# Kernel optimization log

Hardware: AMD Instinct MI355X
Metric: run time of the kernel (lower is better)

Reference implementation:

```python
import jax, jax.numpy as jnp
import numpy as np

L, H, E, DK, FF, V, BS = 6, 16, 1024, 64, 4096, 32000, 1024
B, T = 2, 1024
EPS = 1e-5


def _ln(x, g, b):
    mu = jnp.mean(x, axis=-1, keepdims=True)
    var = jnp.mean(jnp.square(x - mu), axis=-1, keepdims=True)
    return (x - mu) * jax.lax.rsqrt(var + EPS) * g + b


def setup_inputs() -> dict:
    key = jax.random.key(0)
    ks = jax.random.split(key, 12)
    s = 0.02
    return {
        'idx': jax.random.randint(ks[0], (B, T), 0, V),
        'emb': jax.random.normal(ks[1], (V, E), jnp.float32) * s,
        'pos': jax.random.normal(ks[2], (BS, E), jnp.float32) * s,
        'Wq': jax.random.normal(ks[3], (L, H, E, DK), jnp.float32) * s,
        'Wk': jax.random.normal(ks[4], (L, H, E, DK), jnp.float32) * s,
        'Wv': jax.random.normal(ks[5], (L, H, E, DK), jnp.float32) * s,
        'Wp': jax.random.normal(ks[6], (L, E, E), jnp.float32) * s,
        'bp': jnp.zeros((L, E), jnp.float32),
        'ln1_g': jnp.ones((L, E), jnp.float32),
        'ln1_b': jnp.zeros((L, E), jnp.float32),
        'ln2_g': jnp.ones((L, E), jnp.float32),
        'ln2_b': jnp.zeros((L, E), jnp.float32),
        'W1': jax.random.normal(ks[7], (L, E, FF), jnp.float32) * s,
        'b1': jnp.zeros((L, FF), jnp.float32),
        'W2': jax.random.normal(ks[8], (L, FF, E), jnp.float32) * s,
        'b2': jnp.zeros((L, E), jnp.float32),
        'lnf_g': jnp.ones((E,), jnp.float32),
        'lnf_b': jnp.zeros((E,), jnp.float32),
        'Wout': jax.random.normal(ks[9], (E, V), jnp.float32) * s,
        'bout': jnp.zeros((V,), jnp.float32),
    }


def reference(idx, emb, pos, Wq, Wk, Wv, Wp, bp, ln1_g, ln1_b, ln2_g, ln2_b,
              W1, b1, W2, b2, lnf_g, lnf_b, Wout, bout):
    Tcur = idx.shape[1]
    x = emb[idx] + pos[:Tcur]  # [B,T,E]
    # NOTE: original code scales by 1/sqrt(n_embd) (input dim), NOT 1/sqrt(d_k)
    scale = 1.0 / jnp.sqrt(jnp.float32(E))
    causal = jnp.tril(jnp.ones((Tcur, Tcur), bool))
    neg_inf = jnp.float32(-jnp.inf)
    for l in range(L):
        h = _ln(x, ln1_g[l], ln1_b[l])
        q = jnp.einsum('bte,hed->bhtd', h, Wq[l])
        k = jnp.einsum('bte,hed->bhtd', h, Wk[l])
        v = jnp.einsum('bte,hed->bhtd', h, Wv[l])
        scores = jnp.einsum('bhtd,bhsd->bhts', q, k) * scale
        scores = jnp.where(causal, scores, neg_inf)
        attn = jax.nn.softmax(scores, axis=-1)
        o = jnp.einsum('bhts,bhsd->bhtd', attn, v)
        o = o.transpose(0, 2, 1, 3).reshape(x.shape[0], Tcur, H * DK)
        x = x + o @ Wp[l] + bp[l]
        h = _ln(x, ln2_g[l], ln2_b[l])
        x = x + jax.nn.relu(h @ W1[l] + b1[l]) @ W2[l] + b2[l]
    x = _ln(x, lnf_g, lnf_b)
    logits = x @ Wout + bout  # [B,T,V]
    return logits
```

## Files before the change

### kernel.cpp

```cpp
#include <hip/hip_runtime.h>
#include <cstdio>
#include <cstdint>

typedef unsigned short u16;
typedef __bf16 bf16x8 __attribute__((ext_vector_type(8)));
typedef float f32x4 __attribute__((ext_vector_type(4)));

static const int EE = 1024;
static const int TT = 1024;
static const int BB = 2;
static const int NTOK = 2048;
static const int HH = 16;
static const int DK = 64;
static const int FF = 4096;
static const int VV = 32000;
static const int LL = 6;

__device__ __forceinline__ float bf2f(u16 u) {
  unsigned int i = ((unsigned int)u) << 16;
  float f; __builtin_memcpy(&f, &i, 4); return f;
}
__device__ __forceinline__ u16 f2bf(float f) {
  unsigned int i; __builtin_memcpy(&i, &f, 4);
  unsigned int r = i + 0x7fffu + ((i >> 16) & 1u);
  return (u16)(r >> 16);
}

__device__ __forceinline__ void gll16(const u16* g, u16* l) {
  __builtin_amdgcn_global_load_lds(
      (__attribute__((address_space(1))) void*)(uintptr_t)g,
      (__attribute__((address_space(3))) void*)l,
      16, 0, 0);
}

__global__ __launch_bounds__(256) void embed_k(const int* __restrict__ idx,
                                               const float* __restrict__ emb,
                                               const float* __restrict__ pos,
                                               float* __restrict__ x) {
  long i = (long)blockIdx.x * 256 + threadIdx.x;
  int n = (int)(i >> 10), e = (int)(i & 1023);
  int tok = idx[n];
  int t = n & (TT - 1);
  x[i] = emb[(long)tok * EE + e] + pos[(long)t * EE + e];
}

template <int NS>
__global__ __launch_bounds__(256) void ln_fused_k(float* __restrict__ x,
                                                  const float* __restrict__ part, long pstride,
                                                  const float* __restrict__ bias,
                                                  const float* __restrict__ g,
                                                  const float* __restrict__ b,
                                                  u16* __restrict__ out) {
  int row = blockIdx.x * 4 + (threadIdx.x >> 6);
  int lane = threadIdx.x & 63;
  long base = (long)row * EE;
  float v[16];
  float s = 0.f, s2 = 0.f;
#pragma unroll
  for (int j = 0; j < 16; j++) {
    int c = j * 64 + lane;
    float t = x[base + c];
    if constexpr (NS > 0) {
      t += bias[c];
#pragma unroll
      for (int p = 0; p < NS; p++) t += part[(long)p * pstride + base + c];
      x[base + c] = t;
    }
    v[j] = t; s += t; s2 += t * t;
  }
#pragma unroll
  for (int o = 32; o; o >>= 1) { s += __shfl_xor(s, o); s2 += __shfl_xor(s2, o); }
  float mu = s * (1.f / EE);
  float var = s2 * (1.f / EE) - mu * mu;
  float rs = rsqrtf(var + 1e-5f);
  u16* orow = out + base;
#pragma unroll
  for (int j = 0; j < 16; j++) {
    int c = j * 64 + lane;
    orow[c] = f2bf((v[j] - mu) * rs * g[c] + b[c]);
  }
}

__global__ __launch_bounds__(256) void pack_qkvT_k(const float* __restrict__ Wq,
                                                   const float* __restrict__ Wk,
                                                   const float* __restrict__ Wv,
                                                   u16* __restrict__ out) {
  int l = blockIdx.y;
  const float* Wq_l = Wq + (size_t)l * HH * EE * DK;
  const float* Wk_l = Wk + (size_t)l * HH * EE * DK;
  const float* Wv_l = Wv + (size_t)l * HH * EE * DK;
  u16* out_l = out + (size_t)l * 3 * EE * EE;
  long base = ((long)blockIdx.x * 256 + threadIdx.x) * 4;
  int c = (int)(base >> 10);
  int e0 = (int)(base & 1023);
  const float* W = (c < 1024) ? Wq_l : (c < 2048 ? Wk_l : Wv_l);
  int cm = c & 1023;
  int hh = cm >> 6, d = cm & 63;
#pragma unroll
  for (int i = 0; i < 4; i++) {
    int e = e0 + i;
    out_l[(long)c * EE + e] = f2bf(W[((long)hh * EE + e) * DK + d]);
  }
}

template <typename ST>
__global__ __launch_bounds__(256) void transpose_to_bf16(const ST* __restrict__ src,
                                                         long s_z1, long s_z2, int zmod, int ld_s,
                                                         u16* __restrict__ dst,
                                                         long d_z, int ld_d, int R, int C) {
  __shared__ u16 t[32][33];
  int z = blockIdx.z;
  const ST* S = src + (z / zmod) * s_z1 + (z % zmod) * s_z2;
  u16* D = dst + (long)z * d_z;
  int c0 = blockIdx.x * 32, r0 = blockIdx.y * 32;
  int lx = threadIdx.x & 31, ly = threadIdx.x >> 5;
#pragma unroll
  for (int i = 0; i < 4; i++) {
    int r = r0 + ly + i * 8;
    ST val = S[(long)r * ld_s + c0 + lx];
    if constexpr (sizeof(ST) == 4) t[ly + i * 8][lx] = f2bf((float)val);
    else t[ly + i * 8][lx] = (u16)val;
  }
  __syncthreads();
#pragma unroll
  for (int i = 0; i < 4; i++) {
    int c = c0 + ly + i * 8;
    D[(long)c * ld_d + r0 + lx] = t[lx][ly + i * 8];
  }
}

__global__ __launch_bounds__(256) void flash_attn_k(const u16* __restrict__ qkv,
                                                    const u16* __restrict__ vT,
                                                    u16* __restrict__ o) {
  __shared__ u16 Qs[128 * 72];
  __shared__ u16 Ks[2][64 * 72];
  __shared__ u16 Vs[2][64 * 72];
  __shared__ u16 Ps[4][32 * 72];

  int tid = threadIdx.x;
  int lane = tid & 63, w = tid >> 6;
  int fr = lane & 15, kg = lane >> 4;
  int q0 = blockIdx.x * 128;
  int z = blockIdx.y;
  int b = z >> 4, h = z & 15;
  const u16* qbase = qkv + (long)b * TT * 3072 + h * 64;
  const u16* kbase = qbase + 1024;
  const u16* vbase = vT + (long)z * DK * TT;
  const float scale = 0.03125f;

  int4 qreg[4], kreg[2], vreg[2];
#pragma unroll
  for (int i = 0; i < 4; i++) {
    int c = i * 256 + tid, row = c >> 3, c8 = c & 7;
    qreg[i] = *(const int4*)(qbase + (long)(q0 + row) * 3072 + c8 * 8);
  }
#pragma unroll
  for (int i = 0; i < 2; i++) {
    int c = i * 256 + tid, row = c >> 3, c8 = c & 7;
    kreg[i] = *(const int4*)(kbase + (long)row * 3072 + c8 * 8);
    vreg[i] = *(const int4*)(vbase + (long)row * TT + c8 * 8);
  }
#pragma unroll
  for (int i = 0; i < 4; i++) {
    int c = i * 256 + tid, row = c >> 3, c8 = c & 7;
    *(int4*)&Qs[row * 72 + c8 * 8] = qreg[i];
  }
#pragma unroll
  for (int i = 0; i < 2; i++) {
    int c = i * 256 + tid, row = c >> 3, c8 = c & 7;
    *(int4*)&Ks[0][row * 72 + c8 * 8] = kreg[i];
    *(int4*)&Vs[0][row * 72 + c8 * 8] = vreg[i];
  }
  __syncthreads();

  f32x4 zero = {0.f, 0.f, 0.f, 0.f};
  f32x4 acc_o[2][4];
  float m_i[2][4], l_i[2][4];
#pragma unroll
  for (int m = 0; m < 2; m++)
#pragma unroll
    for (int n = 0; n < 4; n++) acc_o[m][n] = zero;
#pragma unroll
  for (int m = 0; m < 2; m++)
#pragma unroll
    for (int r = 0; r < 4; r++) { m_i[m][r] = -1e30f; l_i[m][r] = 0.f; }

  int nt = q0 / 64 + 2;
  for (int t = 0; t < nt; t++) {
    int cur = t & 1;
    int kv0 = t * 64;
    bool pf = (t + 1 < nt);
    if (pf) {
      int kvn = kv0 + 64;
#pragma unroll
      for (int i = 0; i < 2; i++) {
        int c = i * 256 + tid, row = c >> 3, c8 = c & 7;
        kreg[i] = *(const int4*)(kbase + (long)(kvn + row) * 3072 + c8 * 8);
        vreg[i] = *(const int4*)(vbase + (long)row * TT + kvn + c8 * 8);
      }
    }

    f32x4 s[2][4];
#pragma unroll
    for (int m = 0; m < 2; m++)
#pragma unroll
      for (int n = 0; n < 4; n++) s[m][n] = zero;
    {
      bf16x8 aq[2][2], bk[4][2];
#pragma unroll
      for (int m = 0; m < 2; m++)
#pragma unroll
        for (int kk = 0; kk < 2; kk++)
          aq[m][kk] = *(const bf16x8*)&Qs[(w * 32 + m * 16 + fr) * 72 + kk * 32 + kg * 8];
#pragma unroll
      for (int n = 0; n < 4; n++)
#pragma unroll
        for (int kk = 0; kk < 2; kk++)
          bk[n][kk] = *(const bf16x8*)&Ks[cur][(n * 16 + fr) * 72 + kk * 32 + kg * 8];
#pragma unroll
      for (int kk = 0; kk < 2; kk++)
#pragma unroll
        for (int m = 0; m < 2; m++)
#pragma unroll
          for (int n = 0; n < 4; n++)
            s[m][n] = __builtin_amdgcn_mfma_f32_16x16x32_bf16(aq[m][kk], bk[n][kk], s[m][n], 0, 0, 0);
    }

    float sv[2][4][4];
#pragma unroll
    for (int m = 0; m < 2; m++) {
#pragma unroll
      for (int n = 0; n < 4; n++) {
#pragma unroll
        for (int r = 0; r < 4; r++) {
          int qg = q0 + w * 32 + m * 16 + kg * 4 + r;
          int kgl = kv0 + n * 16 + fr;
          float val = s[m][n][r] * scale;
          sv[m][n][r] = (kgl > qg) ? -1e30f : val;
        }
      }
    }
#pragma unroll
    for (int m = 0; m < 2; m++) {
#pragma unroll
      for (int r = 0; r < 4; r++) {
        float rm = fmaxf(fmaxf(sv[m][0][r], sv[m][1][r]), fmaxf(sv[m][2][r], sv[m][3][r]));
        rm = fmaxf(rm, __shfl_xor(rm, 1));
        rm = fmaxf(rm, __shfl_xor(rm, 2));
        rm = fmaxf(rm, __shfl_xor(rm, 4));
        rm = fmaxf(rm, __shfl_xor(rm, 8));
        float mn = fmaxf(m_i[m][r], rm);
        float f = __expf(m_i[m][r] - mn);
        m_i[m][r] = mn;
        float rs = 0.f;
#pragma unroll
        for (int n = 0; n < 4; n++) {
          float p = __expf(sv[m][n][r] - mn);
          sv[m][n][r] = p;
          rs += p;
        }
        rs += __shfl_xor(rs, 1);
        rs += __shfl_xor(rs, 2);
        rs += __shfl_xor(rs, 4);
        rs += __shfl_xor(rs, 8);
        l_i[m][r] = l_i[m][r] * f + rs;
#pragma unroll
        for (int n = 0; n < 4; n++) acc_o[m][n][r] *= f;
      }
    }
#pragma unroll
    for (int m = 0; m < 2; m++)
#pragma unroll
      for (int n = 0; n < 4; n++)
#pragma unroll
        for (int r = 0; r < 4; r++)
          Ps[w][(m * 16 + kg * 4 + r) * 72 + n * 16 + fr] = f2bf(sv[m][n][r]);

    {
      bf16x8 pa[2][2], bv[4][2];
#pragma unroll
      for (int m = 0; m < 2; m++)
#pragma unroll
        for (int kk = 0; kk < 2; kk++)
          pa[m][kk] = *(const bf16x8*)&Ps[w][(m * 16 + fr) * 72 + kk * 32 + kg * 8];
#pragma unroll
      for (int n = 0; n < 4; n++)
#pragma unroll
        for (int kk = 0; kk < 2; kk++)
          bv[n][kk] = *(const bf16x8*)&Vs[cur][(n * 16 + fr) * 72 + kk * 32 + kg * 8];
#pragma unroll
      for (int kk = 0; kk < 2; kk++)
#pragma unroll
        for (int m = 0; m < 2; m++)
#pragma unroll
          for (int n = 0; n < 4; n++)
            acc_o[m][n] = __builtin_amdgcn_mfma_f32_16x16x32_bf16(pa[m][kk], bv[n][kk], acc_o[m][n], 0, 0, 0);
    }

    if (pf) {
#pragma unroll
      for (int i = 0; i < 2; i++) {
        int c = i * 256 + tid, row = c >> 3, c8 = c & 7;
        *(int4*)&Ks[cur ^ 1][row * 72 + c8 * 8] = kreg[i];
        *(int4*)&Vs[cur ^ 1][row * 72 + c8 * 8] = vreg[i];
      }
    }
    __syncthreads();
  }

  u16* obase = o + ((long)b * TT + q0) * EE + h * 64;
#pragma unroll
  for (int m = 0; m < 2; m++) {
#pragma unroll
    for (int r = 0; r < 4; r++) {
      float inv = 1.f / l_i[m][r];
      int qrow = w * 32 + m * 16 + kg * 4 + r;
#pragma unroll
      for (int n = 0; n < 4; n++)
        obase[(long)qrow * EE + n * 16 + fr] = f2bf(acc_o[m][n][r] * inv);
    }
  }
}

template <int EPI>
__global__ __launch_bounds__(256) void gemm_nt(
    const u16* __restrict__ A, const u16* __restrict__ BT, void* Cv,
    const float* __restrict__ bias,
    int Kc, int lda, int ldb, int ldc, long c_zs) {
  constexpr int BK = 64;
  __shared__ u16 As[128 * BK];
  __shared__ u16 Bs[128 * BK];

  int m0 = blockIdx.x * 128, n0 = blockIdx.y * 128;
  int z = blockIdx.z;
  int tid = threadIdx.x, lane = tid & 63, wave = tid >> 6;
  int wm = wave >> 1, wn = wave & 1;
  int fr = lane & 15, kg = lane >> 4;
  int xk0 = ((kg) ^ (fr & 7)) * 8;
  int xk1 = ((4 + kg) ^ (fr & 7)) * 8;

  f32x4 zero = {0.f, 0.f, 0.f, 0.f};
  f32x4 acc[4][4];
#pragma unroll
  for (int m = 0; m < 4; m++)
#pragma unroll
    for (int n = 0; n < 4; n++) acc[m][n] = zero;

  int kbeg = z * Kc;
  for (int k0 = kbeg; k0 < kbeg + Kc; k0 += BK) {
#pragma unroll
    for (int i = 0; i < 4; i++) {
      int c = i * 256 + tid, row = c >> 3;
      int ch = (c & 7) ^ (row & 7);
      gll16(A + (long)(m0 + row) * lda + k0 + ch * 8, &As[c * 8]);
      gll16(BT + (long)(n0 + row) * ldb + k0 + ch * 8, &Bs[c * 8]);
    }
    __syncthreads();
#pragma unroll
    for (int kk = 0; kk < 2; kk++) {
      int xo = kk ? xk1 : xk0;
      bf16x8 af[4], bf[4];
#pragma unroll
      for (int m = 0; m < 4; m++)
        af[m] = *(const bf16x8*)&As[(wm * 64 + m * 16 + fr) * BK + xo];
#pragma unroll
      for (int n = 0; n < 4; n++)
        bf[n] = *(const bf16x8*)&Bs[(wn * 64 + n * 16 + fr) * BK + xo];
#pragma unroll
      for (int m = 0; m < 4; m++)
#pragma unroll
        for (int n = 0; n < 4; n++)
          acc[m][n] = __builtin_amdgcn_mfma_f32_16x16x32_bf16(af[m], bf[n], acc[m][n], 0, 0, 0);
    }
    __syncthreads();
  }

  u16* C16 = (u16*)Cv;
  float* C32 = (float*)Cv;
  long cb = (long)z * c_zs;
  int rowb = m0 + wm * 64, colb = n0 + wn * 64;
#pragma unroll
  for (int m = 0; m < 4; m++) {
#pragma unroll
    for (int n = 0; n < 4; n++) {
      int gc = colb + n * 16 + fr;
      float bv = 0.f;
      if (EPI == 1 || EPI == 2) bv = bias[gc];
#pragma unroll
      for (int r = 0; r < 4; r++) {
        int gr = rowb + m * 16 + kg * 4 + r;
        long ci = cb + (long)gr * ldc + gc;
        float val = acc[m][n][r];
        if (EPI == 0) C16[ci] = f2bf(val);
        else if (EPI == 1) C32[ci] = val + bv;
        else if (EPI == 2) C16[ci] = f2bf(fmaxf(val + bv, 0.f));
        else C32[ci] = val;
      }
    }
  }
}

extern "C" void kernel_launch(void* const* d_in, const int* in_sizes, int n_in,
                              void* d_out, int out_size, void* d_ws, size_t ws_size,
                              hipStream_t stream) {
  const int*   idx  = (const int*)d_in[0];
  const float* emb  = (const float*)d_in[1];
  const float* pos  = (const float*)d_in[2];
  const float* Wq   = (const float*)d_in[3];
  const float* Wk   = (const float*)d_in[4];
  const float* Wv   = (const float*)d_in[5];
  const float* Wp   = (const float*)d_in[6];
  const float* bp   = (const float*)d_in[7];
  const float* ln1g = (const float*)d_in[8];
  const float* ln1b = (const float*)d_in[9];
  const float* ln2g = (const float*)d_in[10];
  const float* ln2b = (const float*)d_in[11];
  const float* W1   = (const float*)d_in[12];
  const float* b1   = (const float*)d_in[13];
  const float* W2   = (const float*)d_in[14];
  const float* b2   = (const float*)d_in[15];
  const float* lnfg = (const float*)d_in[16];
  const float* lnfb = (const float*)d_in[17];
  const float* Wout = (const float*)d_in[18];
  const float* bout = (const float*)d_in[19];

  char* w = (char*)d_ws;
  size_t off = 0;
  auto alloc = [&](size_t bytes) {
    void* p = w + off;
    off += (bytes + 255) & ~(size_t)255;
    return p;
  };
  float* x    = (float*)alloc((size_t)NTOK * EE * 4);
  u16* h      = (u16*)alloc((size_t)NTOK * EE * 2);
  u16* qkv    = (u16*)alloc((size_t)NTOK * 3 * EE * 2);
  u16* vT     = (u16*)alloc((size_t)BB * HH * DK * TT * 2);
  u16* big    = (u16*)alloc((size_t)VV * EE * 2);
  u16* o      = (u16*)alloc((size_t)NTOK * EE * 2);
  u16* mid    = (u16*)alloc((size_t)NTOK * FF * 2);
  u16* W1T    = (u16*)alloc((size_t)FF * EE * 2);
  u16* W2T    = (u16*)alloc((size_t)EE * FF * 2);
  float* pbuf = (float*)alloc((size_t)4 * NTOK * EE * 4);
  if (off > ws_size) {
    fprintf(stderr, "kernel_launch: ws too small, need %zu have %zu\n", off, ws_size);
    return;
  }
  u16* WqkvT_all = big;
  u16* WpT_all   = big + (size_t)6 * 3 * EE * EE;
  const long PS = (long)NTOK * EE;

  embed_k<<<NTOK * EE / 256, 256, 0, stream>>>(idx, emb, pos, x);
  pack_qkvT_k<<<dim3(3 * EE * EE / 1024, LL), 256, 0, stream>>>(Wq, Wk, Wv, WqkvT_all);
  transpose_to_bf16<float><<<dim3(32, 32, LL), 256, 0, stream>>>(
      Wp, (long)EE * EE, 0, 1, EE, WpT_all, (long)EE * EE, EE, EE, EE);

  for (int l = 0; l < LL; l++) {
    if (l == 0)
      ln_fused_k<0><<<NTOK / 4, 256, 0, stream>>>(x, nullptr, 0, nullptr,
                                                  ln1g, ln1b, h);
    else
      ln_fused_k<4><<<NTOK / 4, 256, 0, stream>>>(x, pbuf, PS, b2 + (l - 1) * EE,
                                                  ln1g + l * EE, ln1b + l * EE, h);
    gemm_nt<0><<<dim3(16, 24, 1), 256, 0, stream>>>(
        h, WqkvT_all + (size_t)l * 3 * EE * EE, qkv, nullptr,
        EE, EE, EE, 3 * EE, 0);
    transpose_to_bf16<u16><<<dim3(2, 32, 32), 256, 0, stream>>>(
        qkv + 2 * EE, (long)TT * 3 * EE, 64, 16, 3 * EE,
        vT, (long)DK * TT, TT, TT, DK);
    flash_attn_k<<<dim3(8, 32), 256, 0, stream>>>(qkv, vT, o);
    gemm_nt<4><<<dim3(16, 8, 2), 256, 0, stream>>>(
        o, WpT_all + (size_t)l * EE * EE, pbuf, nullptr,
        512, EE, EE, EE, PS);
    ln_fused_k<2><<<NTOK / 4, 256, 0, stream>>>(x, pbuf, PS, bp + l * EE,
                                                ln2g + l * EE, ln2b + l * EE, h);
    transpose_to_bf16<float><<<dim3(FF / 32, EE / 32, 1), 256, 0, stream>>>(
        W1 + (size_t)l * EE * FF, 0, 0, 1, FF, W1T, 0, EE, EE, FF);
    gemm_nt<2><<<dim3(16, 32, 1), 256, 0, stream>>>(
        h, W1T, mid, b1 + l * FF,
        EE, EE, EE, FF, 0);
    transpose_to_bf16<float><<<dim3(EE / 32, FF / 32, 1), 256, 0, stream>>>(
        W2 + (size_t)l * FF * EE, 0, 0, 1, EE, W2T, 0, FF, FF, EE);
    gemm_nt<4><<<dim3(16, 8, 4), 256, 0, stream>>>(
        mid, W2T, pbuf, nullptr,
        1024, FF, FF, EE, PS);
  }

  ln_fused_k<4><<<NTOK / 4, 256, 0, stream>>>(x, pbuf, PS, b2 + 5 * EE, lnfg, lnfb, h);
  u16* WoutT = big;
  transpose_to_bf16<float><<<dim3(VV / 32, EE / 32, 1), 256, 0, stream>>>(
      Wout, 0, 0, 1, VV, WoutT, 0, EE, EE, VV);
  gemm_nt<1><<<dim3(16, 250, 1), 256, 0, stream>>>(
      h, WoutT, d_out, bout,
      EE, EE, EE, VV, 0);
}
```

Baseline: 1.500 ms.

## Balance causal attention with paired 64-row query tiles and add 256x256 logits GEMM

The flash attention kernel now uses 64-row query tiles. Each block processes two tiles, jq and 15-jq, so every block does about the same amount of causal work instead of late query blocks dominating. The final vocabulary projection moves to a new 512-thread GEMM with 256x256 tiles. That GEMM uses direct global-to-LDS loads into a double buffer, an XOR-swizzled LDS layout and raised MFMA priority, to improve data reuse on the largest matmul. The trade-offs are a large LDS footprint per block, which limits occupancy, and smaller per-wave attention tiles, which give less MFMA work per Q load.

```diff
diff --git a/kernel.cpp b/kernel.cpp
--- a/kernel.cpp
+++ b/kernel.cpp
@@ -132,15 +132,14 @@
 __global__ __launch_bounds__(256) void flash_attn_k(const u16* __restrict__ qkv,
                                                     const u16* __restrict__ vT,
                                                     u16* __restrict__ o) {
-  __shared__ u16 Qs[128 * 72];
+  __shared__ u16 Qs[64 * 72];
   __shared__ u16 Ks[2][64 * 72];
   __shared__ u16 Vs[2][64 * 72];
-  __shared__ u16 Ps[4][32 * 72];
+  __shared__ u16 Ps[4][16 * 72];
 
   int tid = threadIdx.x;
   int lane = tid & 63, w = tid >> 6;
   int fr = lane & 15, kg = lane >> 4;
-  int q0 = blockIdx.x * 128;
   int z = blockIdx.y;
   int b = z >> 4, h = z & 15;
   const u16* qbase = qkv + (long)b * TT * 3072 + h * 64;
@@ -148,176 +147,147 @@
   const u16* vbase = vT + (long)z * DK * TT;
   const float scale = 0.03125f;
 
-  int4 qreg[4], kreg[2], vreg[2];
-#pragma unroll
-  for (int i = 0; i < 4; i++) {
-    int c = i * 256 + tid, row = c >> 3, c8 = c & 7;
-    qreg[i] = *(const int4*)(qbase + (long)(q0 + row) * 3072 + c8 * 8);
-  }
-#pragma unroll
-  for (int i = 0; i < 2; i++) {
-    int c = i * 256 + tid, row = c >> 3, c8 = c & 7;
-    kreg[i] = *(const int4*)(kbase + (long)row * 3072 + c8 * 8);
-    vreg[i] = *(const int4*)(vbase + (long)row * TT + c8 * 8);
-  }
-#pragma unroll
-  for (int i = 0; i < 4; i++) {
-    int c = i * 256 + tid, row = c >> 3, c8 = c & 7;
-    *(int4*)&Qs[row * 72 + c8 * 8] = qreg[i];
-  }
-#pragma unroll
-  for (int i = 0; i < 2; i++) {
-    int c = i * 256 + tid, row = c >> 3, c8 = c & 7;
-    *(int4*)&Ks[0][row * 72 + c8 * 8] = kreg[i];
-    *(int4*)&Vs[0][row * 72 + c8 * 8] = vreg[i];
-  }
-  __syncthreads();
-
-  f32x4 zero = {0.f, 0.f, 0.f, 0.f};
-  f32x4 acc_o[2][4];
-  float m_i[2][4], l_i[2][4];
-#pragma unroll
-  for (int m = 0; m < 2; m++)
-#pragma unroll
-    for (int n = 0; n < 4; n++) acc_o[m][n] = zero;
-#pragma unroll
-  for (int m = 0; m < 2; m++)
-#pragma unroll
-    for (int r = 0; r < 4; r++) { m_i[m][r] = -1e30f; l_i[m][r] = 0.f; }
-
-  int nt = q0 / 64 + 2;
-  for (int t = 0; t < nt; t++) {
-    int cur = t & 1;
-    int kv0 = t * 64;
-    bool pf = (t + 1 < nt);
-    if (pf) {
-      int kvn = kv0 + 64;
-#pragma unroll
-      for (int i = 0; i < 2; i++) {
-        int c = i * 256 + tid, row = c >> 3, c8 = c & 7;
-        kreg[i] = *(const int4*)(kbase + (long)(kvn + row) * 3072 + c8 * 8);
-        vreg[i] = *(const int4*)(vbase + (long)row * TT + kvn + c8 * 8);
-      }
-    }
-
-    f32x4 s[2][4];
-#pragma unroll
-    for (int m = 0; m < 2; m++)
-#pragma unroll
-      for (int n = 0; n < 4; n++) s[m][n] = zero;
-    {
-      bf16x8 aq[2][2], bk[4][2];
-#pragma unroll
-      for (int m = 0; m < 2; m++)
+  for (int p = 0; p < 2; p++) {
+    int jq = (p == 0) ? (int)blockIdx.x : 15 - (int)blockIdx.x;
+    int q0 = jq * 64;
+    int nt = jq + 1;
+    if (p) __syncthreads();
+
+    int4 kreg[2], vreg[2];
+#pragma unroll
+    for (int i = 0; i < 2; i++) {
+      int c = i * 256 + tid, row = c >> 3, c8 = c & 7;
+      *(int4*)&Qs[row * 72 + c8 * 8] = *(const int4*)(qbase + (long)(q0 + row) * 3072 + c8 * 8);
+      kreg[i] = *(const int4*)(kbase + (long)row * 3072 + c8 * 8);
+      vreg[i] = *(const int4*)(vbase + (long)row * TT + c8 * 8);
+    }
+#pragma unroll
+    for (int i = 0; i < 2; i++) {
+      int c = i * 256 + tid, row = c >> 3, c8 = c & 7;
+      *(int4*)&Ks[0][row * 72 + c8 * 8] = kreg[i];
+      *(int4*)&Vs[0][row * 72 + c8 * 8] = vreg[i];
+    }
+    __syncthreads();
+
+    f32x4 zero = {0.f, 0.f, 0.f, 0.f};
+    f32x4 acc_o[4];
+    float m_i[4], l_i[4];
+#pragma unroll
+    for (int n = 0; n < 4; n++) acc_o[n] = zero;
+#pragma unroll
+    for (int r = 0; r < 4; r++) { m_i[r] = -1e30f; l_i[r] = 0.f; }
+
+    for (int t = 0; t < nt; t++) {
+      int cur = t & 1;
+      int kv0 = t * 64;
+      bool pf = (t + 1 < nt);
+      if (pf) {
+        int kvn = kv0 + 64;
+#pragma unroll
+        for (int i = 0; i < 2; i++) {
+          int c = i * 256 + tid, row = c >> 3, c8 = c & 7;
+          kreg[i] = *(const int4*)(kbase + (long)(kvn + row) * 3072 + c8 * 8);
+          vreg[i] = *(const int4*)(vbase + (long)row * TT + kvn + c8 * 8);
+        }
+      }
+
+      f32x4 s[4];
+#pragma unroll
+      for (int n = 0; n < 4; n++) s[n] = zero;
+      {
+        bf16x8 aq[2], bk[4][2];
 #pragma unroll
         for (int kk = 0; kk < 2; kk++)
-          aq[m][kk] = *(const bf16x8*)&Qs[(w * 32 + m * 16 + fr) * 72 + kk * 32 + kg * 8];
+          aq[kk] = *(const bf16x8*)&Qs[(w * 16 + fr) * 72 + kk * 32 + kg * 8];
+#pragma unroll
+        for (int n = 0; n < 4; n++)
+#pragma unroll
+          for (int kk = 0; kk < 2; kk++)
+            bk[n][kk] = *(const bf16x8*)&Ks[cur][(n * 16 + fr) * 72 + kk * 32 + kg * 8];
+#pragma unroll
+        for (int kk = 0; kk < 2; kk++)
+#pragma unroll
+          for (int n = 0; n < 4; n++)
+            s[n] = __builtin_amdgcn_mfma_f32_16x16x32_bf16(aq[kk], bk[n][kk], s[n], 0, 0, 0);
+      }
+
+      float sv[4][4];
 #pragma unroll
       for (int n = 0; n < 4; n++)
 #pragma unroll
-        for (int kk = 0; kk < 2; kk++)
-          bk[n][kk] = *(const bf16x8*)&Ks[cur][(n * 16 + fr) * 72 + kk * 32 + kg * 8];
-#pragma unroll
-      for (int kk = 0; kk < 2; kk++)
-#pragma unroll
-        for (int m = 0; m < 2; m++)
-#pragma unroll
-          for (int n = 0; n < 4; n++)
-            s[m][n] = __builtin_amdgcn_mfma_f32_16x16x32_bf16(aq[m][kk], bk[n][kk], s[m][n], 0, 0, 0);
-    }
-
-    float sv[2][4][4];
-#pragma unroll
-    for (int m = 0; m < 2; m++) {
-#pragma unroll
-      for (int n = 0; n < 4; n++) {
-#pragma unroll
         for (int r = 0; r < 4; r++) {
-          int qg = q0 + w * 32 + m * 16 + kg * 4 + r;
+          int qg = q0 + w * 16 + kg * 4 + r;
           int kgl = kv0 + n * 16 + fr;
-          float val = s[m][n][r] * scale;
-          sv[m][n][r] = (kgl > qg) ? -1e30f : val;
+          float val = s[n][r] * scale;
+          sv[n][r] = (kgl > qg) ? -1e30f : val;
         }
-      }
-    }
-#pragma unroll
-    for (int m = 0; m < 2; m++) {
 #pragma unroll
       for (int r = 0; r < 4; r++) {
-        float rm = fmaxf(fmaxf(sv[m][0][r], sv[m][1][r]), fmaxf(sv[m][2][r], sv[m][3][r]));
+        float rm = fmaxf(fmaxf(sv[0][r], sv[1][r]), fmaxf(sv[2][r], sv[3][r]));
         rm = fmaxf(rm, __shfl_xor(rm, 1));
         rm = fmaxf(rm, __shfl_xor(rm, 2));
         rm = fmaxf(rm, __shfl_xor(rm, 4));
         rm = fmaxf(rm, __shfl_xor(rm, 8));
-        float mn = fmaxf(m_i[m][r], rm);
-        float f = __expf(m_i[m][r] - mn);
-        m_i[m][r] = mn;
+        float mn = fmaxf(m_i[r], rm);
+        float f = __expf(m_i[r] - mn);
+        m_i[r] = mn;
         float rs = 0.f;
 #pragma unroll
         for (int n = 0; n < 4; n++) {
-          float p = __expf(sv[m][n][r] - mn);
-          sv[m][n][r] = p;
-          rs += p;
+          float pv = __expf(sv[n][r] - mn);
+          sv[n][r] = pv;
+          rs += pv;
         }
         rs += __shfl_xor(rs, 1);
         rs += __shfl_xor(rs, 2);
         rs += __shfl_xor(rs, 4);
         rs += __shfl_xor(rs, 8);
-        l_i[m][r] = l_i[m][r] * f + rs;
-#pragma unroll
-        for (int n = 0; n < 4; n++) acc_o[m][n][r] *= f;
-      }
-    }
-#pragma unroll
-    for (int m = 0; m < 2; m++)
+        l_i[r] = l_i[r] * f + rs;
+#pragma unroll
+        for (int n = 0; n < 4; n++) acc_o[n][r] *= f;
+      }
 #pragma unroll
       for (int n = 0; n < 4; n++)
 #pragma unroll
         for (int r = 0; r < 4; r++)
-          Ps[w][(m * 16 + kg * 4 + r) * 72 + n * 16 + fr] = f2bf(sv[m][n][r]);
-
-    {
-      bf16x8 pa[2][2], bv[4][2];
-#pragma unroll
-      for (int m = 0; m < 2; m++)
+          Ps[w][(kg * 4 + r) * 72 + n * 16 + fr] = f2bf(sv[n][r]);
+
+      {
+        bf16x8 pa[2], bv[4][2];
 #pragma unroll
         for (int kk = 0; kk < 2; kk++)
-          pa[m][kk] = *(const bf16x8*)&Ps[w][(m * 16 + fr) * 72 + kk * 32 + kg * 8];
+          pa[kk] = *(const bf16x8*)&Ps[w][fr * 72 + kk * 32 + kg * 8];
+#pragma unroll
+        for (int n = 0; n < 4; n++)
+#pragma unroll
+          for (int kk = 0; kk < 2; kk++)
+            bv[n][kk] = *(const bf16x8*)&Vs[cur][(n * 16 + fr) * 72 + kk * 32 + kg * 8];
+#pragma unroll
+        for (int kk = 0; kk < 2; kk++)
+#pragma unroll
+          for (int n = 0; n < 4; n++)
+            acc_o[n] = __builtin_amdgcn_mfma_f32_16x16x32_bf16(pa[kk], bv[n][kk], acc_o[n], 0, 0, 0);
+      }
+
+      if (pf) {
+#pragma unroll
+        for (int i = 0; i < 2; i++) {
+          int c = i * 256 + tid, row = c >> 3, c8 = c & 7;
+          *(int4*)&Ks[cur ^ 1][row * 72 + c8 * 8] = kreg[i];
+          *(int4*)&Vs[cur ^ 1][row * 72 + c8 * 8] = vreg[i];
+        }
+      }
+      __syncthreads();
+    }
+
+    u16* obase = o + ((long)b * TT + q0) * EE + h * 64;
+#pragma unroll
+    for (int r = 0; r < 4; r++) {
+      float inv = 1.f / l_i[r];
+      int qrow = w * 16 + kg * 4 + r;
 #pragma unroll
       for (int n = 0; n < 4; n++)
-#pragma unroll
-        for (int kk = 0; kk < 2; kk++)
-          bv[n][kk] = *(const bf16x8*)&Vs[cur][(n * 16 + fr) * 72 + kk * 32 + kg * 8];
-#pragma unroll
-      for (int kk = 0; kk < 2; kk++)
-#pragma unroll
-        for (int m = 0; m < 2; m++)
-#pragma unroll
-          for (int n = 0; n < 4; n++)
-            acc_o[m][n] = __builtin_amdgcn_mfma_f32_16x16x32_bf16(pa[m][kk], bv[n][kk], acc_o[m][n], 0, 0, 0);
-    }
-
-    if (pf) {
-#pragma unroll
-      for (int i = 0; i < 2; i++) {
-        int c = i * 256 + tid, row = c >> 3, c8 = c & 7;
-        *(int4*)&Ks[cur ^ 1][row * 72 + c8 * 8] = kreg[i];
-        *(int4*)&Vs[cur ^ 1][row * 72 + c8 * 8] = vreg[i];
-      }
-    }
-    __syncthreads();
-  }
-
-  u16* obase = o + ((long)b * TT + q0) * EE + h * 64;
-#pragma unroll
-  for (int m = 0; m < 2; m++) {
-#pragma unroll
-    for (int r = 0; r < 4; r++) {
-      float inv = 1.f / l_i[m][r];
-      int qrow = w * 32 + m * 16 + kg * 4 + r;
-#pragma unroll
-      for (int n = 0; n < 4; n++)
-        obase[(long)qrow * EE + n * 16 + fr] = f2bf(acc_o[m][n][r] * inv);
+        obase[(long)qrow * EE + n * 16 + fr] = f2bf(acc_o[n][r] * inv);
     }
   }
 }
@@ -395,6 +365,103 @@
         else if (EPI == 1) C32[ci] = val + bv;
         else if (EPI == 2) C16[ci] = f2bf(fmaxf(val + bv, 0.f));
         else C32[ci] = val;
+      }
+    }
+  }
+}
+
+__global__ __launch_bounds__(512) void gemm256_nt(
+    const u16* __restrict__ A, const u16* __restrict__ BT,
+    float* __restrict__ C, const float* __restrict__ bias,
+    int K, int lda, int ldb, int ldc) {
+  __shared__ u16 lds[2][2][256 * 64];
+
+  int tid = threadIdx.x, lane = tid & 63, wave = tid >> 6;
+  int wm = wave >> 2, wn = wave & 3;
+  int fr = lane & 15, kg = lane >> 4;
+  int m0 = blockIdx.x * 256, n0 = blockIdx.y * 256;
+
+  auto STAGE = [&](int t, int b) {
+    int k0 = t * 64;
+#pragma unroll
+    for (int r = 0; r < 4; r++) {
+      int g = r * 512 + tid;
+      int row = g >> 3, cl = (g & 7) ^ (row & 7);
+      gll16(A + (long)(m0 + row) * lda + k0 + cl * 8, &lds[b][0][g * 8]);
+    }
+#pragma unroll
+    for (int r = 0; r < 4; r++) {
+      int g = r * 512 + tid;
+      int row = g >> 3, cl = (g & 7) ^ (row & 7);
+      gll16(BT + (long)(n0 + row) * ldb + k0 + cl * 8, &lds[b][1][g * 8]);
+    }
+  };
+
+  f32x4 zero = {0.f, 0.f, 0.f, 0.f};
+  f32x4 acc[8][4];
+#pragma unroll
+  for (int m = 0; m < 8; m++)
+#pragma unroll
+    for (int n = 0; n < 4; n++) acc[m][n] = zero;
+
+  int NT = K / 64;
+  STAGE(0, 0);
+  if (NT > 1) STAGE(1, 1);
+
+  for (int c = 0; c < NT; c++) {
+    if (c + 1 < NT) asm volatile("s_waitcnt vmcnt(8)" ::: "memory");
+    else            asm volatile("s_waitcnt vmcnt(0)" ::: "memory");
+    __builtin_amdgcn_s_barrier();
+    const u16* Ab = lds[c & 1][0];
+    const u16* Bb = lds[c & 1][1];
+#pragma unroll
+    for (int ph = 0; ph < 4; ph++) {
+      int mh = ph >> 1, nh = ph & 1;
+      bf16x8 af[4][2], bf[2][2];
+#pragma unroll
+      for (int m = 0; m < 4; m++) {
+        int row = wm * 128 + mh * 64 + m * 16 + fr;
+#pragma unroll
+        for (int kk = 0; kk < 2; kk++) {
+          int cp = (kk * 4 + kg) ^ (row & 7);
+          af[m][kk] = *(const bf16x8*)&Ab[row * 64 + cp * 8];
+        }
+      }
+#pragma unroll
+      for (int n = 0; n < 2; n++) {
+        int row = wn * 64 + nh * 32 + n * 16 + fr;
+#pragma unroll
+        for (int kk = 0; kk < 2; kk++) {
+          int cp = (kk * 4 + kg) ^ (row & 7);
+          bf[n][kk] = *(const bf16x8*)&Bb[row * 64 + cp * 8];
+        }
+      }
+      __builtin_amdgcn_s_setprio(1);
+#pragma unroll
+      for (int kk = 0; kk < 2; kk++)
+#pragma unroll
+        for (int m = 0; m < 4; m++)
+#pragma unroll
+          for (int n = 0; n < 2; n++)
+            acc[mh * 4 + m][nh * 2 + n] = __builtin_amdgcn_mfma_f32_16x16x32_bf16(
+                af[m][kk], bf[n][kk], acc[mh * 4 + m][nh * 2 + n], 0, 0, 0);
+      __builtin_amdgcn_s_setprio(0);
+    }
+    __builtin_amdgcn_s_barrier();
+    if (c + 2 < NT) STAGE(c + 2, c & 1);
+  }
+
+  int rowb = m0 + wm * 128, colb = n0 + wn * 64;
+#pragma unroll
+  for (int m = 0; m < 8; m++) {
+#pragma unroll
+    for (int n = 0; n < 4; n++) {
+      int gc = colb + n * 16 + fr;
+      float bv = bias[gc];
+#pragma unroll
+      for (int r = 0; r < 4; r++) {
+        int gr = rowb + m * 16 + kg * 4 + r;
+        C[(long)gr * ldc + gc] = acc[m][n][r] + bv;
       }
     }
   }
@@ -489,7 +556,6 @@
   u16* WoutT = big;
   transpose_to_bf16<float><<<dim3(VV / 32, EE / 32, 1), 256, 0, stream>>>(
       Wout, 0, 0, 1, VV, WoutT, 0, EE, EE, VV);
-  gemm_nt<1><<<dim3(16, 250, 1), 256, 0, stream>>>(
-      h, WoutT, d_out, bout,
-      EE, EE, EE, VV, 0);
-}
+  gemm256_nt<<<dim3(NTOK / 256, VV / 256, 1), 512, 0, stream>>>(
+      h, WoutT, (float*)d_out, bout, EE, EE, EE, VV);
+}
```

New measurement: 1.383 ms. 1.08x faster.
